# Optimization experiments

Hardware: AMD Instinct MI355X
Metric: run time of the kernel (lower is better)

Reference implementation:

```python
import jax, jax.numpy as jnp
import numpy as np

N, H = 8192, 1024

def setup_inputs() -> dict:
    key = jax.random.key(0)
    ks = jax.random.split(key, 7)
    s = 1.0 / np.sqrt(H)
    return {
        "input_tensor": jax.random.normal(ks[0], (N, H), dtype=jnp.float32),
        "Wq": jax.random.uniform(ks[1], (H, H), dtype=jnp.float32, minval=-s, maxval=s),
        "bq": jax.random.uniform(ks[2], (H,), dtype=jnp.float32, minval=-s, maxval=s),
        "Wk": jax.random.uniform(ks[3], (H, H), dtype=jnp.float32, minval=-s, maxval=s),
        "bk": jax.random.uniform(ks[4], (H,), dtype=jnp.float32, minval=-s, maxval=s),
        "Wv": jax.random.uniform(ks[5], (H, H), dtype=jnp.float32, minval=-s, maxval=s),
        "bv": jax.random.uniform(ks[6], (H,), dtype=jnp.float32, minval=-s, maxval=s),
    }

def reference(input_tensor, Wq, bq, Wk, bk, Wv, bv):
    # torch nn.Linear: x @ W.T + b
    q = input_tensor @ Wq.T + bq  # [N, H]
    k = input_tensor @ Wk.T + bk  # [N, H]
    v = input_tensor @ Wv.T + bv  # [N, H]
    scale = jnp.sqrt(jnp.asarray(input_tensor.shape[1], dtype=q.dtype))
    # (q @ k.T / sqrt(H)) @ v  -- no softmax; same math as original
    scores = (q @ k.T) / scale  # [N, N]
    return scores @ v  # [N, H]
```

## Files before the change

### kernel.cpp

```cpp
#include <hip/hip_runtime.h>
#include <hip/hip_bf16.h>
#include <stdint.h>
#include <stddef.h>

typedef __bf16 bf16_t;
typedef __bf16 bf16x4 __attribute__((ext_vector_type(4)));
typedef __bf16 bf16x8 __attribute__((ext_vector_type(8)));
typedef float  floatx4 __attribute__((ext_vector_type(4)));

#define TK 32

__global__ void prep_x(const float* __restrict__ x, bf16_t* __restrict__ xb,
                       bf16_t* __restrict__ xbT, float* __restrict__ s,
                       int SEQ, int H) {
    __shared__ bf16_t tile[64][72];
    __shared__ float csum[64];
    const int t = threadIdx.x;
    const int n0 = blockIdx.x * 64, k0 = blockIdx.y * 64;
    const int c4 = t & 15;
    const int rbase = t >> 4;
    float a0 = 0.f, a1 = 0.f, a2 = 0.f, a3 = 0.f;
    if (t < 64) csum[t] = 0.f;
    #pragma unroll
    for (int p = 0; p < 4; ++p) {
        const int r = rbase + 16 * p;
        const size_t gidx = (size_t)(n0 + r) * H + k0 + c4 * 4;
        float4 f = *(const float4*)(x + gidx);
        bf16x4 o;
        o.x = (bf16_t)f.x; o.y = (bf16_t)f.y;
        o.z = (bf16_t)f.z; o.w = (bf16_t)f.w;
        *(bf16x4*)(xb + gidx) = o;
        *(bf16x4*)&tile[r][c4 * 4] = o;
        a0 += f.x; a1 += f.y; a2 += f.z; a3 += f.w;
    }
    __syncthreads();
    atomicAdd(&csum[c4 * 4 + 0], a0);
    atomicAdd(&csum[c4 * 4 + 1], a1);
    atomicAdd(&csum[c4 * 4 + 2], a2);
    atomicAdd(&csum[c4 * 4 + 3], a3);
    #pragma unroll
    for (int p = 0; p < 2; ++p) {
        const int q = t + 256 * p;
        const int kk = q >> 3;
        const int n8 = (q & 7) * 8;
        bf16x8 v;
        #pragma unroll
        for (int u = 0; u < 8; ++u) v[u] = tile[n8 + u][kk];
        *(bf16x8*)(xbT + (size_t)(k0 + kk) * SEQ + n0 + n8) = v;
    }
    __syncthreads();
    if (t < 64) atomicAdd(s + k0 + t, csum[t]);
}

__global__ void prep_w(const float* __restrict__ Wk, bf16_t* __restrict__ Wkb,
                       const float* __restrict__ Wv, bf16_t* __restrict__ Wvb,
                       const float* __restrict__ Wq, bf16_t* __restrict__ WqTb,
                       float* __restrict__ svec) {
    __shared__ bf16_t tile[64][72];
    const int b = blockIdx.x;
    const int t = threadIdx.x;
    if (b == 2304) {
        *(float4*)(svec + t * 4) = float4{0.f, 0.f, 0.f, 0.f};
        return;
    }
    if (b < 2048) {
        const float* s = (b < 1024) ? Wk : Wv;
        bf16_t* d = (b < 1024) ? Wkb : Wvb;
        const int base = (b & 1023) * 1024 + t * 4;
        float4 f = *(const float4*)(s + base);
        bf16x4 o;
        o.x = (bf16_t)f.x; o.y = (bf16_t)f.y;
        o.z = (bf16_t)f.z; o.w = (bf16_t)f.w;
        *(bf16x4*)(d + base) = o;
    } else {
        const int bb = b - 2048;
        const int r0 = (bb & 15) * 64, c0 = (bb >> 4) * 64;
        const int c4 = t & 15;
        const int rbase = t >> 4;
        #pragma unroll
        for (int p = 0; p < 4; ++p) {
            const int r = rbase + 16 * p;
            float4 f = *(const float4*)(Wq + (size_t)(r0 + r) * 1024 + c0 + c4 * 4);
            bf16x4 o;
            o.x = (bf16_t)f.x; o.y = (bf16_t)f.y;
            o.z = (bf16_t)f.z; o.w = (bf16_t)f.w;
            *(bf16x4*)&tile[r][c4 * 4] = o;
        }
        __syncthreads();
        #pragma unroll
        for (int p = 0; p < 2; ++p) {
            const int q = t + 256 * p;
            const int cc = q >> 3;
            const int r8 = (q & 7) * 8;
            bf16x8 v;
            #pragma unroll
            for (int u = 0; u < 8; ++u) v[u] = tile[r8 + u][cc];
            *(bf16x8*)(WqTb + (size_t)(c0 + cc) * 1024 + r0 + r8) = v;
        }
    }
}

__global__ void reduce_bf16(const bf16_t* __restrict__ part,
                            bf16_t* __restrict__ dst, int n, int nsplit,
                            float scale) {
    int i = (blockIdx.x * blockDim.x + threadIdx.x) * 8;
    if (i < n) {
        float acc[8] = {};
        for (int z = 0; z < nsplit; ++z) {
            bf16x8 p = *(const bf16x8*)(part + (size_t)z * n + i);
            #pragma unroll
            for (int u = 0; u < 8; ++u) acc[u] += (float)p[u];
        }
        bf16x8 o;
        #pragma unroll
        for (int u = 0; u < 8; ++u) o[u] = (bf16_t)(acc[u] * scale);
        *(bf16x8*)(dst + i) = o;
    }
}

template <int TMp, int TNp, int MODE, int SWZ, int MERGE, typename OutT>
__global__ __launch_bounds__(256, 2) void gemm_bt(
    const bf16_t* __restrict__ A, const bf16_t* __restrict__ B,
    OutT* __restrict__ C, const float* __restrict__ p1,
    int M, int N, int K, int kChunk, float scale, int ngemm,
    const float* __restrict__ e_bv, const float* __restrict__ e_kv1,
    const float* __restrict__ e_wvs, const float* __restrict__ e_bk, float cN,
    const bf16_t* __restrict__ mvM0, const bf16_t* __restrict__ mvM1,
    const float* __restrict__ mvv, float* __restrict__ mvy0,
    float* __restrict__ mvy1, float mvScale)
{
    const int tid = threadIdx.x;
    const int L = blockIdx.x;

    if (MERGE && L >= ngemm) {
        const int lane = tid & 63, wv = tid >> 6;
        #pragma unroll
        for (int rr = 0; rr < ((MERGE == 1) ? 2 : 1); ++rr) {
            const bf16_t* mp;
            float* y;
            if (MERGE == 1) {
                const int row = (L - ngemm) * 8 + wv * 2 + rr;
                if (row >= 1024) { mp = mvM1 + (size_t)(row - 1024) * 1024; y = mvy1 + row - 1024; }
                else             { mp = mvM0 + (size_t)row * 1024;          y = mvy0 + row; }
            } else {
                const int row = (L - ngemm) * 4 + wv;
                mp = mvM0 + (size_t)row * 1024;
                y = mvy0 + row;
            }
            float acc = 0.f;
            for (int a = lane * 8; a < 1024; a += 512) {
                bf16x8 m8 = *(const bf16x8*)(mp + a);
                #pragma unroll
                for (int u = 0; u < 8; ++u) acc += (float)m8[u] * mvv[a + u];
            }
            #pragma unroll
            for (int off = 32; off; off >>= 1) acc += __shfl_down(acc, off);
            if (lane == 0) *y = acc * mvScale;
        }
        return;
    }

    __shared__ __align__(16) bf16_t As[TMp * TK];
    __shared__ __align__(16) bf16_t Bs[TNp * TK];
    constexpr int MF = TMp / 32;
    constexpr int NF = TNp / 32;
    constexpr int nA = TMp / 64;
    constexpr int nB = TNp / 64;

    const int lane = tid & 63;
    const int wave = tid >> 6;
    const int wm   = wave >> 1;
    const int wn   = wave & 1;

    int bm, bn, z;
    if (SWZ == 1) {
        z = ((L & 7) << 1) | (L >> 9);
        const int mn = (L >> 3) & 63;
        bm = (mn >> 3) * TMp; bn = (mn & 7) * TNp;
    } else if (SWZ == 2) {
        bm = ((L & 7) * 8 + ((L >> 3) & 7)) * TMp;
        bn = (L >> 6) * TNp;
        z = 0;
    } else {
        bm = (L >> 4) * TMp;
        bn = (L & 15) * TNp;
        z = 0;
    }
    const int k0 = z * kChunk;
    C += (size_t)z * M * N;

    floatx4 acc[MF][NF] = {};
    const int fr = lane & 15;
    const int fk = (lane >> 4) * 8;

    for (int kt = k0; kt < k0 + kChunk; kt += TK) {
        #pragma unroll
        for (int p = 0; p < nA; ++p) {
            const int c = tid + 256 * p;
            const int r = c >> 2, o = (c & 3) * 8;
            __builtin_amdgcn_global_load_lds(
                (const __attribute__((address_space(1))) void*)
                    (A + (size_t)(bm + r) * K + kt + o),
                (__attribute__((address_space(3))) void*)&As[c * 8], 16, 0, 0);
        }
        #pragma unroll
        for (int p = 0; p < nB; ++p) {
            const int c = tid + 256 * p;
            const int r = c >> 2, o = (c & 3) * 8;
            __builtin_amdgcn_global_load_lds(
                (const __attribute__((address_space(1))) void*)
                    (B + (size_t)(bn + r) * K + kt + o),
                (__attribute__((address_space(3))) void*)&Bs[c * 8], 16, 0, 0);
        }
        __syncthreads();

        bf16x8 af[MF], bg[NF];
        #pragma unroll
        for (int i = 0; i < MF; ++i)
            af[i] = *(const bf16x8*)&As[(wm * (TMp / 2) + i * 16 + fr) * TK + fk];
        #pragma unroll
        for (int j = 0; j < NF; ++j)
            bg[j] = *(const bf16x8*)&Bs[(wn * (TNp / 2) + j * 16 + fr) * TK + fk];
        #pragma unroll
        for (int i = 0; i < MF; ++i) {
            #pragma unroll
            for (int j = 0; j < NF; ++j) {
                acc[i][j] = __builtin_amdgcn_mfma_f32_16x16x32_bf16(
                    af[i], bg[j], acc[i][j], 0, 0, 0);
            }
        }
        __syncthreads();
    }

    const int rq = (lane >> 4) * 4;
    #pragma unroll
    for (int i = 0; i < MF; ++i) {
        #pragma unroll
        for (int j = 0; j < NF; ++j) {
            const int col = bn + wn * (TNp / 2) + j * 16 + fr;
            #pragma unroll
            for (int r = 0; r < 4; ++r) {
                const int row = bm + wm * (TMp / 2) + i * 16 + rq + r;
                float v = acc[i][j][r] * scale;
                if (MODE == 1) v += p1[col];
                if (MODE == 2)
                    v += e_bv[row] * e_kv1[col] + (e_wvs[row] + cN * e_bv[row]) * e_bk[col];
                C[(size_t)row * N + col] = (OutT)v;
            }
        }
    }
}

extern "C" void kernel_launch(void* const* d_in, const int* in_sizes, int n_in,
                              void* d_out, int out_size, void* d_ws, size_t ws_size,
                              hipStream_t stream) {
    const int SEQ = 8192;
    const int H   = 1024;

    const float* x  = (const float*)d_in[0];
    const float* Wq = (const float*)d_in[1];
    const float* bq = (const float*)d_in[2];
    const float* Wk = (const float*)d_in[3];
    const float* bk = (const float*)d_in[4];
    const float* Wv = (const float*)d_in[5];
    const float* bv = (const float*)d_in[6];
    float* out = (float*)d_out;

    const size_t MI = 1024 * 1024;
    char* ws = (char*)d_ws;
    bf16_t* xb   = (bf16_t*)(ws);
    bf16_t* xbT  = (bf16_t*)(ws + 16 * MI);
    bf16_t* Wkb  = (bf16_t*)(ws + 32 * MI);
    bf16_t* Wvb  = (bf16_t*)(ws + 34 * MI);
    bf16_t* WqTb = (bf16_t*)(ws + 36 * MI);
    bf16_t* Gb   = (bf16_t*)(ws + 38 * MI);
    bf16_t* S1b  = (bf16_t*)(ws + 40 * MI);
    bf16_t* Ttb  = (bf16_t*)(ws + 42 * MI);
    bf16_t* Utb  = (bf16_t*)(ws + 44 * MI);
    float*  svec = (float*)(ws + 46 * MI);
    float*  kv1  = svec + 1024;
    float*  wvs  = svec + 2048;
    float*  cvec = svec + 3072;
    bf16_t* part = (bf16_t*)(ws + 48 * MI);

    dim3 blk(256);
    const float inv32 = 1.0f / 32.0f;
    const int nHH = H * H;
    const int rgrid = nHH / 8 / 256;
    const float* nf = nullptr;
    const bf16_t* nb = nullptr;
    float* nfm = nullptr;

    prep_w<<<dim3(2305), blk, 0, stream>>>(Wk, Wkb, Wv, Wvb, Wq, WqTb, svec);
    prep_x<<<dim3(SEQ / 64, H / 64), blk, 0, stream>>>(x, xb, xbT, svec, SEQ, H);
    gemm_bt<128, 128, 0, 1, 1, bf16_t><<<dim3(1280), blk, 0, stream>>>(
        xbT, xbT, part, nf, H, H, SEQ, SEQ / 16, 1.0f, 1024,
        nf, nf, nf, nf, 0.f, Wkb, Wvb, svec, kv1, wvs, 1.0f);
    reduce_bf16<<<dim3(rgrid), blk, 0, stream>>>(part, Gb, nHH, 16, 1.0f);
    gemm_bt<64, 64, 0, 4, 0, bf16_t><<<dim3(256), blk, 0, stream>>>(
        Wvb, Gb, S1b, nf, H, H, H, H, 1.0f, 1 << 30,
        nf, nf, nf, nf, 0.f, nb, nb, nf, nfm, nfm, 0.f);
    gemm_bt<64, 64, 2, 4, 0, bf16_t><<<dim3(256), blk, 0, stream>>>(
        S1b, Wkb, Ttb, nf, H, H, H, H, 1.0f, 1 << 30,
        bv, kv1, wvs, bk, (float)SEQ, nb, nb, nf, nfm, nfm, 0.f);
    gemm_bt<64, 64, 0, 4, 2, bf16_t><<<dim3(512), blk, 0, stream>>>(
        Ttb, WqTb, Utb, nf, H, H, H, H, inv32, 256,
        nf, nf, nf, nf, 0.f, Ttb, nb, bq, cvec, nfm, inv32);
    gemm_bt<128, 128, 1, 2, 0, float><<<dim3(512), blk, 0, stream>>>(
        xb, Utb, out, cvec, SEQ, H, H, H, 1.0f, 1 << 30,
        nf, nf, nf, nf, 0.f, nb, nb, nf, nfm, nfm, 0.f);
}
```

Before: 212.0 us.

## Precompute Wq^T·Wk product in prep stage to remove one dependent HxH GEMM

Reassociates the weight chain so that Wq^T·Wk (W2) is computed during the x-prep kernel, overlapping with the x cast/transpose work. This removes one serial 1024^3 GEMM launch from the critical path. The bias correction terms are folded into the new matrix-vector merge paths and epilogue via extra dot products (r1, r2, q1). In exchange it adds a transposed Wk copy and more complex epilogue math, and bf16 rounding happens at different points.

```diff
diff --git a/kernel.cpp b/kernel.cpp
--- a/kernel.cpp
+++ b/kernel.cpp
@@ -10,13 +10,136 @@
 
 #define TK 32
 
-__global__ void prep_x(const float* __restrict__ x, bf16_t* __restrict__ xb,
-                       bf16_t* __restrict__ xbT, float* __restrict__ s,
-                       int SEQ, int H) {
+__global__ void prep_w(const float* __restrict__ Wk, bf16_t* __restrict__ Wkb,
+                       bf16_t* __restrict__ WkTb,
+                       const float* __restrict__ Wv, bf16_t* __restrict__ Wvb,
+                       const float* __restrict__ Wq, bf16_t* __restrict__ WqTb,
+                       float* __restrict__ svec) {
     __shared__ bf16_t tile[64][72];
-    __shared__ float csum[64];
+    const int b = blockIdx.x;
     const int t = threadIdx.x;
-    const int n0 = blockIdx.x * 64, k0 = blockIdx.y * 64;
+    if (b == 1536) {
+        *(float4*)(svec + t * 4) = float4{0.f, 0.f, 0.f, 0.f};
+        return;
+    }
+    if (b >= 512) {
+        const int base = (b - 512) * 1024 + t * 4;
+        float4 f = *(const float4*)(Wv + base);
+        bf16x4 o;
+        o.x = (bf16_t)f.x; o.y = (bf16_t)f.y;
+        o.z = (bf16_t)f.z; o.w = (bf16_t)f.w;
+        *(bf16x4*)(Wvb + base) = o;
+        return;
+    }
+    const bool isK = (b < 256);
+    const int bb = b & 255;
+    const float* src = isK ? Wk : Wq;
+    bf16_t* dT = isK ? WkTb : WqTb;
+    const int r0 = (bb >> 4) * 64, c0 = (bb & 15) * 64;
+    const int c4 = t & 15;
+    const int rbase = t >> 4;
+    #pragma unroll
+    for (int p = 0; p < 4; ++p) {
+        const int r = rbase + 16 * p;
+        const size_t gidx = (size_t)(r0 + r) * 1024 + c0 + c4 * 4;
+        float4 f = *(const float4*)(src + gidx);
+        bf16x4 o;
+        o.x = (bf16_t)f.x; o.y = (bf16_t)f.y;
+        o.z = (bf16_t)f.z; o.w = (bf16_t)f.w;
+        if (isK) *(bf16x4*)(Wkb + gidx) = o;
+        *(bf16x4*)&tile[r][c4 * 4] = o;
+    }
+    __syncthreads();
+    #pragma unroll
+    for (int p = 0; p < 2; ++p) {
+        const int q = t + 256 * p;
+        const int cc = q >> 3;
+        const int r8 = (q & 7) * 8;
+        bf16x8 v;
+        #pragma unroll
+        for (int u = 0; u < 8; ++u) v[u] = tile[r8 + u][cc];
+        *(bf16x8*)(dT + (size_t)(c0 + cc) * 1024 + r0 + r8) = v;
+    }
+}
+
+__global__ void prep_x_fused(const float* __restrict__ x,
+                             bf16_t* __restrict__ xb, bf16_t* __restrict__ xbT,
+                             float* __restrict__ svec,
+                             const bf16_t* __restrict__ WqTb,
+                             const bf16_t* __restrict__ WkTb,
+                             bf16_t* __restrict__ W2Tb,
+                             const float* __restrict__ bq,
+                             float* __restrict__ q1, int SEQ, int H) {
+    __shared__ __align__(16) char smem[9472];
+    const int L = blockIdx.x;
+    const int t = threadIdx.x;
+    if (L < 256) {
+        bf16_t* As = (bf16_t*)smem;
+        bf16_t* Bs = (bf16_t*)(smem + 4096);
+        const int bm = (L >> 4) * 64, bn = (L & 15) * 64;
+        const int lane = t & 63, wave = t >> 6;
+        const int wm = wave >> 1, wn = wave & 1;
+        floatx4 acc[2][2] = {};
+        const int fr = lane & 15, fk = (lane >> 4) * 8;
+        const int sr = t >> 2, so = (t & 3) * 8;
+        for (int kt = 0; kt < 1024; kt += TK) {
+            __builtin_amdgcn_global_load_lds(
+                (const __attribute__((address_space(1))) void*)
+                    (WqTb + (size_t)(bm + sr) * 1024 + kt + so),
+                (__attribute__((address_space(3))) void*)&As[t * 8], 16, 0, 0);
+            __builtin_amdgcn_global_load_lds(
+                (const __attribute__((address_space(1))) void*)
+                    (WkTb + (size_t)(bn + sr) * 1024 + kt + so),
+                (__attribute__((address_space(3))) void*)&Bs[t * 8], 16, 0, 0);
+            __syncthreads();
+            bf16x8 af[2], bg[2];
+            #pragma unroll
+            for (int i = 0; i < 2; ++i)
+                af[i] = *(const bf16x8*)&As[(wm * 32 + i * 16 + fr) * TK + fk];
+            #pragma unroll
+            for (int j = 0; j < 2; ++j)
+                bg[j] = *(const bf16x8*)&Bs[(wn * 32 + j * 16 + fr) * TK + fk];
+            #pragma unroll
+            for (int i = 0; i < 2; ++i)
+                #pragma unroll
+                for (int j = 0; j < 2; ++j)
+                    acc[i][j] = __builtin_amdgcn_mfma_f32_16x16x32_bf16(
+                        af[i], bg[j], acc[i][j], 0, 0, 0);
+            __syncthreads();
+        }
+        const int rq = (lane >> 4) * 4;
+        #pragma unroll
+        for (int i = 0; i < 2; ++i)
+            #pragma unroll
+            for (int j = 0; j < 2; ++j) {
+                const int col = bn + wn * 32 + j * 16 + fr;
+                #pragma unroll
+                for (int r = 0; r < 4; ++r) {
+                    const int row = bm + wm * 32 + i * 16 + rq + r;
+                    W2Tb[(size_t)row * 1024 + col] = (bf16_t)acc[i][j][r];
+                }
+            }
+        return;
+    }
+    if (L < 512) {
+        const int lane = t & 63, wv = t >> 6;
+        const int row = (L - 256) * 4 + wv;
+        const bf16_t* mp = WkTb + (size_t)row * 1024;
+        float acc = 0.f;
+        for (int a = lane * 8; a < 1024; a += 512) {
+            bf16x8 m8 = *(const bf16x8*)(mp + a);
+            #pragma unroll
+            for (int u = 0; u < 8; ++u) acc += (float)m8[u] * bq[a + u];
+        }
+        #pragma unroll
+        for (int off = 32; off; off >>= 1) acc += __shfl_down(acc, off);
+        if (lane == 0) q1[row] = acc;
+        return;
+    }
+    bf16_t (*tile)[72] = (bf16_t(*)[72])smem;
+    float* csum = (float*)(smem + 9216);
+    const int LL = L - 512;
+    const int n0 = (LL >> 4) * 64, k0 = (LL & 15) * 64;
     const int c4 = t & 15;
     const int rbase = t >> 4;
     float a0 = 0.f, a1 = 0.f, a2 = 0.f, a3 = 0.f;
@@ -49,55 +172,7 @@
         *(bf16x8*)(xbT + (size_t)(k0 + kk) * SEQ + n0 + n8) = v;
     }
     __syncthreads();
-    if (t < 64) atomicAdd(s + k0 + t, csum[t]);
-}
-
-__global__ void prep_w(const float* __restrict__ Wk, bf16_t* __restrict__ Wkb,
-                       const float* __restrict__ Wv, bf16_t* __restrict__ Wvb,
-                       const float* __restrict__ Wq, bf16_t* __restrict__ WqTb,
-                       float* __restrict__ svec) {
-    __shared__ bf16_t tile[64][72];
-    const int b = blockIdx.x;
-    const int t = threadIdx.x;
-    if (b == 2304) {
-        *(float4*)(svec + t * 4) = float4{0.f, 0.f, 0.f, 0.f};
-        return;
-    }
-    if (b < 2048) {
-        const float* s = (b < 1024) ? Wk : Wv;
-        bf16_t* d = (b < 1024) ? Wkb : Wvb;
-        const int base = (b & 1023) * 1024 + t * 4;
-        float4 f = *(const float4*)(s + base);
-        bf16x4 o;
-        o.x = (bf16_t)f.x; o.y = (bf16_t)f.y;
-        o.z = (bf16_t)f.z; o.w = (bf16_t)f.w;
-        *(bf16x4*)(d + base) = o;
-    } else {
-        const int bb = b - 2048;
-        const int r0 = (bb & 15) * 64, c0 = (bb >> 4) * 64;
-        const int c4 = t & 15;
-        const int rbase = t >> 4;
-        #pragma unroll
-        for (int p = 0; p < 4; ++p) {
-            const int r = rbase + 16 * p;
-            float4 f = *(const float4*)(Wq + (size_t)(r0 + r) * 1024 + c0 + c4 * 4);
-            bf16x4 o;
-            o.x = (bf16_t)f.x; o.y = (bf16_t)f.y;
-            o.z = (bf16_t)f.z; o.w = (bf16_t)f.w;
-            *(bf16x4*)&tile[r][c4 * 4] = o;
-        }
-        __syncthreads();
-        #pragma unroll
-        for (int p = 0; p < 2; ++p) {
-            const int q = t + 256 * p;
-            const int cc = q >> 3;
-            const int r8 = (q & 7) * 8;
-            bf16x8 v;
-            #pragma unroll
-            for (int u = 0; u < 8; ++u) v[u] = tile[r8 + u][cc];
-            *(bf16x8*)(WqTb + (size_t)(c0 + cc) * 1024 + r0 + r8) = v;
-        }
-    }
+    if (t < 64) atomicAdd(svec + k0 + t, csum[t]);
 }
 
 __global__ void reduce_bf16(const bf16_t* __restrict__ part,
@@ -126,36 +201,73 @@
     const float* __restrict__ e_bv, const float* __restrict__ e_kv1,
     const float* __restrict__ e_wvs, const float* __restrict__ e_bk, float cN,
     const bf16_t* __restrict__ mvM0, const bf16_t* __restrict__ mvM1,
-    const float* __restrict__ mvv, float* __restrict__ mvy0,
-    float* __restrict__ mvy1, float mvScale)
+    const float* __restrict__ mvv, const float* __restrict__ mvv2,
+    const float* __restrict__ mvv3, const float* __restrict__ mvv4,
+    float* __restrict__ mvy0, float* __restrict__ mvy1, float mvScale)
 {
     const int tid = threadIdx.x;
     const int L = blockIdx.x;
 
     if (MERGE && L >= ngemm) {
         const int lane = tid & 63, wv = tid >> 6;
-        #pragma unroll
-        for (int rr = 0; rr < ((MERGE == 1) ? 2 : 1); ++rr) {
-            const bf16_t* mp;
-            float* y;
-            if (MERGE == 1) {
+        if (MERGE == 1) {
+            #pragma unroll
+            for (int rr = 0; rr < 2; ++rr) {
                 const int row = (L - ngemm) * 8 + wv * 2 + rr;
+                const bf16_t* mp;
+                float* y;
                 if (row >= 1024) { mp = mvM1 + (size_t)(row - 1024) * 1024; y = mvy1 + row - 1024; }
                 else             { mp = mvM0 + (size_t)row * 1024;          y = mvy0 + row; }
-            } else {
-                const int row = (L - ngemm) * 4 + wv;
-                mp = mvM0 + (size_t)row * 1024;
-                y = mvy0 + row;
-            }
-            float acc = 0.f;
+                float acc = 0.f;
+                for (int a = lane * 8; a < 1024; a += 512) {
+                    bf16x8 m8 = *(const bf16x8*)(mp + a);
+                    #pragma unroll
+                    for (int u = 0; u < 8; ++u) acc += (float)m8[u] * mvv[a + u];
+                }
+                #pragma unroll
+                for (int off = 32; off; off >>= 1) acc += __shfl_down(acc, off);
+                if (lane == 0) *y = acc * mvScale;
+            }
+        } else if (MERGE == 3) {
+            const int row = (L - ngemm) * 4 + wv;
+            const bf16_t* mp = mvM0 + (size_t)row * 1024;
+            float s1 = 0.f, s2 = 0.f;
             for (int a = lane * 8; a < 1024; a += 512) {
                 bf16x8 m8 = *(const bf16x8*)(mp + a);
                 #pragma unroll
-                for (int u = 0; u < 8; ++u) acc += (float)m8[u] * mvv[a + u];
-            }
-            #pragma unroll
-            for (int off = 32; off; off >>= 1) acc += __shfl_down(acc, off);
-            if (lane == 0) *y = acc * mvScale;
+                for (int u = 0; u < 8; ++u) {
+                    const float m = (float)m8[u];
+                    s1 += m * mvv[a + u];
+                    s2 += m * mvv2[a + u];
+                }
+            }
+            #pragma unroll
+            for (int off = 32; off; off >>= 1) {
+                s1 += __shfl_down(s1, off);
+                s2 += __shfl_down(s2, off);
+            }
+            if (lane == 0) { mvy0[row] = s1; mvy1[row] = s2; }
+        } else {
+            const int row = (L - ngemm) * 4 + wv;
+            const bf16_t* mp = mvM0 + (size_t)row * 1024;
+            float s0 = 0.f, c1 = 0.f, c2 = 0.f;
+            for (int a = lane * 8; a < 1024; a += 512) {
+                bf16x8 m8 = *(const bf16x8*)(mp + a);
+                #pragma unroll
+                for (int u = 0; u < 8; ++u) {
+                    s0 += (float)m8[u] * mvv[a + u];
+                    c1 += mvv3[a + u] * mvv2[a + u];
+                    c2 += mvv4[a + u] * mvv2[a + u];
+                }
+            }
+            #pragma unroll
+            for (int off = 32; off; off >>= 1) {
+                s0 += __shfl_down(s0, off);
+                c1 += __shfl_down(c1, off);
+                c2 += __shfl_down(c2, off);
+            }
+            if (lane == 0)
+                mvy0[row] = (s0 + e_bv[row] * c1 + (e_wvs[row] + cN * e_bv[row]) * c2) * mvScale;
         }
         return;
     }
@@ -241,10 +353,11 @@
             #pragma unroll
             for (int r = 0; r < 4; ++r) {
                 const int row = bm + wm * (TMp / 2) + i * 16 + rq + r;
-                float v = acc[i][j][r] * scale;
+                float v = acc[i][j][r];
+                if (MODE == 3)
+                    v += e_bv[row] * e_kv1[col] + (e_wvs[row] + cN * e_bv[row]) * e_bk[col];
+                v *= scale;
                 if (MODE == 1) v += p1[col];
-                if (MODE == 2)
-                    v += e_bv[row] * e_kv1[col] + (e_wvs[row] + cN * e_bv[row]) * e_bk[col];
                 C[(size_t)row * N + col] = (OutT)v;
             }
         }
@@ -275,13 +388,17 @@
     bf16_t* WqTb = (bf16_t*)(ws + 36 * MI);
     bf16_t* Gb   = (bf16_t*)(ws + 38 * MI);
     bf16_t* S1b  = (bf16_t*)(ws + 40 * MI);
-    bf16_t* Ttb  = (bf16_t*)(ws + 42 * MI);
+    bf16_t* W2Tb = (bf16_t*)(ws + 42 * MI);
     bf16_t* Utb  = (bf16_t*)(ws + 44 * MI);
     float*  svec = (float*)(ws + 46 * MI);
     float*  kv1  = svec + 1024;
     float*  wvs  = svec + 2048;
     float*  cvec = svec + 3072;
+    float*  q1   = svec + 4096;
+    float*  r1   = svec + 5120;
+    float*  r2   = svec + 6144;
     bf16_t* part = (bf16_t*)(ws + 48 * MI);
+    bf16_t* WkTb = (bf16_t*)(ws + 80 * MI);
 
     dim3 blk(256);
     const float inv32 = 1.0f / 32.0f;
@@ -291,22 +408,20 @@
     const bf16_t* nb = nullptr;
     float* nfm = nullptr;
 
-    prep_w<<<dim3(2305), blk, 0, stream>>>(Wk, Wkb, Wv, Wvb, Wq, WqTb, svec);
-    prep_x<<<dim3(SEQ / 64, H / 64), blk, 0, stream>>>(x, xb, xbT, svec, SEQ, H);
+    prep_w<<<dim3(1537), blk, 0, stream>>>(Wk, Wkb, WkTb, Wv, Wvb, Wq, WqTb, svec);
+    prep_x_fused<<<dim3(2560), blk, 0, stream>>>(
+        x, xb, xbT, svec, WqTb, WkTb, W2Tb, bq, q1, SEQ, H);
     gemm_bt<128, 128, 0, 1, 1, bf16_t><<<dim3(1280), blk, 0, stream>>>(
         xbT, xbT, part, nf, H, H, SEQ, SEQ / 16, 1.0f, 1024,
-        nf, nf, nf, nf, 0.f, Wkb, Wvb, svec, kv1, wvs, 1.0f);
+        nf, nf, nf, nf, 0.f, Wkb, Wvb, svec, nf, nf, nf, kv1, wvs, 1.0f);
     reduce_bf16<<<dim3(rgrid), blk, 0, stream>>>(part, Gb, nHH, 16, 1.0f);
-    gemm_bt<64, 64, 0, 4, 0, bf16_t><<<dim3(256), blk, 0, stream>>>(
-        Wvb, Gb, S1b, nf, H, H, H, H, 1.0f, 1 << 30,
-        nf, nf, nf, nf, 0.f, nb, nb, nf, nfm, nfm, 0.f);
-    gemm_bt<64, 64, 2, 4, 0, bf16_t><<<dim3(256), blk, 0, stream>>>(
-        S1b, Wkb, Ttb, nf, H, H, H, H, 1.0f, 1 << 30,
-        bv, kv1, wvs, bk, (float)SEQ, nb, nb, nf, nfm, nfm, 0.f);
-    gemm_bt<64, 64, 0, 4, 2, bf16_t><<<dim3(512), blk, 0, stream>>>(
-        Ttb, WqTb, Utb, nf, H, H, H, H, inv32, 256,
-        nf, nf, nf, nf, 0.f, Ttb, nb, bq, cvec, nfm, inv32);
+    gemm_bt<64, 64, 0, 4, 3, bf16_t><<<dim3(512), blk, 0, stream>>>(
+        Wvb, Gb, S1b, nf, H, H, H, H, 1.0f, 256,
+        nf, nf, nf, nf, 0.f, WqTb, nb, kv1, bk, nf, nf, r1, r2, 1.0f);
+    gemm_bt<64, 64, 3, 4, 4, bf16_t><<<dim3(512), blk, 0, stream>>>(
+        S1b, W2Tb, Utb, nf, H, H, H, H, inv32, 256,
+        bv, r1, wvs, r2, (float)SEQ, S1b, nb, q1, bq, kv1, bk, cvec, nfm, inv32);
     gemm_bt<128, 128, 1, 2, 0, float><<<dim3(512), blk, 0, stream>>>(
         xb, Utb, out, cvec, SEQ, H, H, H, 1.0f, 1 << 30,
-        nf, nf, nf, nf, 0.f, nb, nb, nf, nfm, nfm, 0.f);
+        nf, nf, nf, nf, 0.f, nb, nb, nf, nf, nf, nf, nfm, nfm, 0.f);
 }
```

New measurement: 199.7 us. -5.8%, faster.
